# Optimization experiments

Hardware: AMD Instinct MI355X
Metric: run time of the kernel (lower is better)

The kernel has to match this reference:

```python
import jax, jax.numpy as jnp
import numpy as np

N_NODES = 100000
N_EDGES = 500000
HIDDEN = 256


def setup_inputs() -> dict:
    key = jax.random.key(0)
    k_x, k_e, k_w1, k_b1, k_w2, k_b2 = jax.random.split(key, 6)
    x = jax.random.normal(k_x, (N_NODES, HIDDEN), dtype=jnp.float32)
    edge_label_index = jax.random.randint(k_e, (2, N_EDGES), 0, N_NODES, dtype=jnp.int64)
    # fc1: Linear(2*hidden -> hidden); fc2: Linear(hidden -> 1). PyTorch stores W as [out, in].
    bound1 = 1.0 / np.sqrt(2 * HIDDEN)
    W1 = jax.random.uniform(k_w1, (HIDDEN, 2 * HIDDEN), dtype=jnp.float32, minval=-bound1, maxval=bound1)
    b1 = jax.random.uniform(k_b1, (HIDDEN,), dtype=jnp.float32, minval=-bound1, maxval=bound1)
    bound2 = 1.0 / np.sqrt(HIDDEN)
    W2 = jax.random.uniform(k_w2, (1, HIDDEN), dtype=jnp.float32, minval=-bound2, maxval=bound2)
    b2 = jax.random.uniform(k_b2, (1,), dtype=jnp.float32, minval=-bound2, maxval=bound2)
    return {"x": x, "edge_label_index": edge_label_index, "W1": W1, "b1": b1, "W2": W2, "b2": b2}


def reference(x, edge_label_index, W1, b1, W2, b2):
    # Gather endpoint features: [E, H] each
    feat_src = x[edge_label_index[0]]
    feat_dst = x[edge_label_index[1]]
    h = jnp.concatenate([feat_src, feat_dst], axis=1)  # [E, 2H]
    h = jax.nn.relu(h @ W1.T + b1)                      # [E, H]
    out = jax.nn.sigmoid(h @ W2.T + b2)                 # [E, 1]
    return out.reshape(-1)
```

## Files before the change

kernel.cpp:

```cpp
#include <hip/hip_runtime.h>
#include <math.h>

#define NNODES 100000
#define MT     64
#define NTILES 1563
#define NODESP (NTILES * MT)
#define NEDGES 500000
#define HID    256
#define K2     512
#define GEMM_GRID 256

typedef _Float16 h8v __attribute__((ext_vector_type(8)));
typedef _Float16 h2v __attribute__((ext_vector_type(2)));
typedef __bf16   bf16x8 __attribute__((ext_vector_type(8)));
typedef float    f32x4  __attribute__((ext_vector_type(4)));

__device__ __forceinline__ unsigned short f2bf(float f) {
    unsigned int u = __float_as_uint(f);
    u += 0x7FFFu + ((u >> 16) & 1u);
    return (unsigned short)(u >> 16);
}

__global__ void cvt_w1h(const float* __restrict__ W1, _Float16* __restrict__ Bsw) {
    int t = blockIdx.x * 256 + threadIdx.x;
    if (t >= 8 * 32 * 64) return;
    int lane = t & 63, nt = (t >> 6) & 31, kt = t >> 11;
    int j = nt * 16 + (lane & 15);
    int k = kt * 32 + ((lane >> 4) << 3);
    const float* src = W1 + (size_t)(j & 255) * K2 + ((j >> 8) << 8) + k;
    union { _Float16 s[8]; uint4 v; } u;
#pragma unroll
    for (int jj = 0; jj < 8; ++jj) u.s[jj] = (_Float16)src[jj];
    ((uint4*)Bsw)[t] = u.v;
}

__global__ void cvt_w2p(const float* __restrict__ W2, float* __restrict__ w2p) {
    int t = threadIdx.x;
    int i = (t >> 2) & 15, nt = t & 3;
    w2p[t] = W2[(t & ~63) | (nt * 16 + i)];
}

__global__ __launch_bounds__(512, 2) void node_gemm4(
    const float* __restrict__ x,
    const _Float16* __restrict__ Bsw,
    const float* __restrict__ b1,
    _Float16* __restrict__ UV)
{
    __shared__ __align__(16) _Float16 Asw[2048 * 8];
    const int tid  = threadIdx.x;
    const int lane = tid & 63;
    const int wave = tid >> 6;

    const h8v* B8 = (const h8v*)Bsw;
    h8v barr[8][4];
#pragma unroll
    for (int ks = 0; ks < 8; ++ks)
#pragma unroll
        for (int nt = 0; nt < 4; ++nt)
            barr[ks][nt] = B8[((size_t)(ks * 32 + wave * 4 + nt)) * 64 + lane];

    float b1v[4];
#pragma unroll
    for (int nt = 0; nt < 4; ++nt) {
        int col = wave * 64 + nt * 16 + (lane & 15);
        b1v[nt] = (col < 256) ? b1[col] : 0.0f;
    }

    uint4* A4 = (uint4*)Asw;
    const h8v* A8 = (const h8v*)Asw;
    const int k8  = tid & 31;
    const int mh  = tid >> 5;
    const int ktl = k8 >> 2, q = k8 & 3;

    auto stage = [&](int tile) {
#pragma unroll
        for (int i = 0; i < 4; ++i) {
            int m   = i * 16 + mh;
            int row = tile * MT + m;
            int rl  = row < NNODES ? row : 0;
            const float4* p = (const float4*)(x + (size_t)rl * 256 + k8 * 8);
            float4 a = p[0], b = p[1];
            union { _Float16 s[8]; uint4 v; } u;
            u.s[0] = (_Float16)a.x; u.s[1] = (_Float16)a.y;
            u.s[2] = (_Float16)a.z; u.s[3] = (_Float16)a.w;
            u.s[4] = (_Float16)b.x; u.s[5] = (_Float16)b.y;
            u.s[6] = (_Float16)b.z; u.s[7] = (_Float16)b.w;
            int logical = (ktl << 8) + ((m >> 4) << 6) + (q << 4) + (m & 15);
            A4[logical ^ ktl] = u.v;
        }
    };

    f32x4 acc[4][4] = {};
    int tile = blockIdx.x;
    if (tile >= NTILES) return;
    stage(tile);
    __syncthreads();

    while (true) {
#pragma unroll
        for (int ks = 0; ks < 8; ++ks) {
            h8v af[4];
#pragma unroll
            for (int mt = 0; mt < 4; ++mt)
                af[mt] = A8[(((ks * 4 + mt) << 6) + lane) ^ ks];
#pragma unroll
            for (int mt = 0; mt < 4; ++mt)
#pragma unroll
                for (int nt = 0; nt < 4; ++nt)
                    acc[mt][nt] = __builtin_amdgcn_mfma_f32_16x16x32_f16(
                        af[mt], barr[ks][nt], acc[mt][nt], 0, 0, 0);
        }
        __syncthreads();

        int next = tile + GEMM_GRID;
        if (next < NTILES) stage(next);

#pragma unroll
        for (int mt = 0; mt < 4; ++mt) {
#pragma unroll
            for (int r = 0; r < 4; ++r) {
                int row = tile * MT + mt * 16 + ((lane >> 4) << 2) + r;
                union { _Float16 h[4]; uint2 v; } pk;
#pragma unroll
                for (int nt = 0; nt < 4; ++nt)
                    pk.h[nt] = (_Float16)(acc[mt][nt][r] + b1v[nt]);
                *(uint2*)(UV + (size_t)row * 512 + wave * 64 + (lane & 15) * 4) = pk.v;
            }
        }
#pragma unroll
        for (int mt = 0; mt < 4; ++mt)
#pragma unroll
            for (int nt = 0; nt < 4; ++nt)
                acc[mt][nt] = f32x4{0.f, 0.f, 0.f, 0.f};

        if (next >= NTILES) break;
        tile = next;
        __syncthreads();
    }
}

__global__ __launch_bounds__(256) void edge_out4(
    const _Float16* __restrict__ UV,
    const int* __restrict__ ei,
    const float* __restrict__ w2p,
    const float* __restrict__ b2,
    float* __restrict__ out)
{
    const int tid = threadIdx.x;
    const int q   = tid & 31;
    const int g   = tid >> 5;
    const long e  = (long)blockIdx.x * 32 + g * 4;

    int4 s4 = *(const int4*)(ei + e);
    int4 d4 = *(const int4*)(ei + NEDGES + e);

    h2v w2h[4];
    {
        const float4* pw = (const float4*)w2p + q * 2;
        float4 c = pw[0], d = pw[1];
        w2h[0] = h2v{(_Float16)c.x, (_Float16)c.y};
        w2h[1] = h2v{(_Float16)c.z, (_Float16)c.w};
        w2h[2] = h2v{(_Float16)d.x, (_Float16)d.y};
        w2h[3] = h2v{(_Float16)d.z, (_Float16)d.w};
    }

    union U8 { uint4 v; h2v h[4]; };
    const _Float16* up = UV + q * 8;

    U8 uu[4], vv[4];
    uu[0].v = *(const uint4*)(up + (size_t)s4.x * 512);
    vv[0].v = *(const uint4*)(up + (size_t)d4.x * 512 + 256);
    uu[1].v = *(const uint4*)(up + (size_t)s4.y * 512);
    vv[1].v = *(const uint4*)(up + (size_t)d4.y * 512 + 256);
    uu[2].v = *(const uint4*)(up + (size_t)s4.z * 512);
    vv[2].v = *(const uint4*)(up + (size_t)d4.z * 512 + 256);
    uu[3].v = *(const uint4*)(up + (size_t)s4.w * 512);
    vv[3].v = *(const uint4*)(up + (size_t)d4.w * 512 + 256);

    const h2v zz = {(_Float16)0.0f, (_Float16)0.0f};
    float z[4] = {0.f, 0.f, 0.f, 0.f};
#pragma unroll
    for (int ed = 0; ed < 4; ++ed) {
#pragma unroll
        for (int p = 0; p < 4; ++p) {
            h2v h = uu[ed].h[p] + vv[ed].h[p];
            h = __builtin_elementwise_max(h, zz);
            z[ed] = __builtin_amdgcn_fdot2(h, w2h[p], z[ed], false);
        }
    }
#pragma unroll
    for (int m = 1; m < 32; m <<= 1) {
        z[0] += __shfl_xor(z[0], m, 32);
        z[1] += __shfl_xor(z[1], m, 32);
        z[2] += __shfl_xor(z[2], m, 32);
        z[3] += __shfl_xor(z[3], m, 32);
    }
    if (q < 4) {
        float zq = (q == 0) ? z[0] : (q == 1) ? z[1] : (q == 2) ? z[2] : z[3];
        out[e + q] = 1.0f / (1.0f + expf(-(zq + b2[0])));
    }
}

__global__ void cvt_w1_r1(const float* __restrict__ W1, unsigned short* __restrict__ Bsw) {
    int t = blockIdx.x * 256 + threadIdx.x;
    if (t >= 16 * 16 * 64) return;
    int lane = t & 63, nt = (t >> 6) & 15, kt = t >> 10;
    int n = nt * 16 + (lane & 15);
    int k = kt * 32 + ((lane >> 4) << 3);
    const float* src = W1 + (size_t)n * K2 + k;
    union { unsigned short s[8]; uint4 v; } u;
#pragma unroll
    for (int j = 0; j < 8; ++j) u.s[j] = f2bf(src[j]);
    ((uint4*)Bsw)[t] = u.v;
}

__global__ __launch_bounds__(256) void edge_mlp_fb(
    const float* __restrict__ xf, const int* __restrict__ ei,
    const unsigned short* __restrict__ Bsw, const float* __restrict__ b1,
    const float* __restrict__ W2, const float* __restrict__ b2,
    float* __restrict__ out)
{
    __shared__ __align__(16) unsigned short Asw[8 * 4 * 64 * 8];
    __shared__ float es[64];
    const int tid = threadIdx.x, lane = tid & 63, wave = tid >> 6;
    const int e0 = blockIdx.x * 64;
    if (tid < 64) es[tid] = 0.0f;
    f32x4 acc[4][4] = {};
    const bf16x8* A8 = (const bf16x8*)Asw;
    const bf16x8* B8 = (const bf16x8*)Bsw;
    for (int h = 0; h < 2; ++h) {
#pragma unroll
        for (int i = 0; i < 8; ++i) {
            int m = i * 8 + wave * 2 + (lane >> 5);
            int e = e0 + m;
            int ee = (e < NEDGES) ? e : 0;
            int node = ei[(size_t)h * NEDGES + ee];
            int chunk = lane & 31;
            const float4* p = (const float4*)(xf + ((size_t)node << 8) + (chunk << 3));
            float4 a = p[0], bq = p[1];
            union { unsigned short s[8]; uint4 v4; } u;
            u.s[0] = f2bf(a.x);  u.s[1] = f2bf(a.y);  u.s[2] = f2bf(a.z);  u.s[3] = f2bf(a.w);
            u.s[4] = f2bf(bq.x); u.s[5] = f2bf(bq.y); u.s[6] = f2bf(bq.z); u.s[7] = f2bf(bq.w);
            int ktl = chunk >> 2, qq = chunk & 3;
            int u16 = ((ktl * 4 + (m >> 4)) << 6) + (qq << 4) + (m & 15);
            u16 ^= (u16 >> 8) & 7;
            ((uint4*)Asw)[u16] = u.v4;
        }
        __syncthreads();
#pragma unroll
        for (int kt = 0; kt < 8; ++kt) {
            bf16x8 af[4], bfr[4];
#pragma unroll
            for (int mt = 0; mt < 4; ++mt) {
                int u16 = ((kt * 4 + mt) << 6) + lane;
                u16 ^= (u16 >> 8) & 7;
                af[mt] = A8[u16];
            }
#pragma unroll
            for (int nt = 0; nt < 4; ++nt)
                bfr[nt] = B8[(((h * 8 + kt) << 4) + (wave << 2) + nt) * 64 + lane];
#pragma unroll
            for (int mt = 0; mt < 4; ++mt)
#pragma unroll
                for (int nt = 0; nt < 4; ++nt)
                    acc[mt][nt] = __builtin_amdgcn_mfma_f32_16x16x32_bf16(
                        af[mt], bfr[nt], acc[mt][nt], 0, 0, 0);
        }
        __syncthreads();
    }
    float w2v[4], b1v[4];
#pragma unroll
    for (int nt = 0; nt < 4; ++nt) {
        int n = (wave << 6) + (nt << 4) + (lane & 15);
        w2v[nt] = W2[n]; b1v[nt] = b1[n];
    }
#pragma unroll
    for (int mt = 0; mt < 4; ++mt) {
#pragma unroll
        for (int r = 0; r < 4; ++r) {
            float p = 0.0f;
#pragma unroll
            for (int nt = 0; nt < 4; ++nt) {
                float hv = acc[mt][nt][r] + b1v[nt];
                p = fmaf(fmaxf(hv, 0.0f), w2v[nt], p);
            }
            p += __shfl_xor(p, 1, 16);
            p += __shfl_xor(p, 2, 16);
            p += __shfl_xor(p, 4, 16);
            p += __shfl_xor(p, 8, 16);
            if ((lane & 15) == 0)
                atomicAdd(&es[(mt << 4) + ((lane >> 4) << 2) + r], p);
        }
    }
    __syncthreads();
    if (tid < 64) {
        int e = e0 + tid;
        if (e < NEDGES) out[e] = 1.0f / (1.0f + expf(-(es[tid] + b2[0])));
    }
}

extern "C" void kernel_launch(void* const* d_in, const int* in_sizes, int n_in,
                              void* d_out, int out_size, void* d_ws, size_t ws_size,
                              hipStream_t stream) {
    const float* x  = (const float*)d_in[0];
    const int*   ei = (const int*)d_in[1];
    const float* W1 = (const float*)d_in[2];
    const float* b1 = (const float*)d_in[3];
    const float* W2 = (const float*)d_in[4];
    const float* b2 = (const float*)d_in[5];
    float* out = (float*)d_out;

    const size_t BSW_BYTES = 1 << 18;
    const size_t W2P_BYTES = 4096;
    const size_t UV_BYTES  = (size_t)NODESP * K2 * 2;
    const size_t NEED_A = BSW_BYTES + W2P_BYTES + UV_BYTES;

    if (ws_size >= NEED_A) {
        _Float16* Bsw = (_Float16*)d_ws;
        float*    w2p = (float*)((char*)d_ws + BSW_BYTES);
        _Float16* UV  = (_Float16*)((char*)d_ws + BSW_BYTES + W2P_BYTES);
        cvt_w1h<<<64, 256, 0, stream>>>(W1, Bsw);
        cvt_w2p<<<1, 256, 0, stream>>>(W2, w2p);
        node_gemm4<<<GEMM_GRID, 512, 0, stream>>>(x, Bsw, b1, UV);
        edge_out4<<<NEDGES / 32, 256, 0, stream>>>(UV, ei, w2p, b2, out);
    } else {
        unsigned short* Bsw = (unsigned short*)d_ws;
        cvt_w1_r1<<<64, 256, 0, stream>>>(W1, Bsw);
        edge_mlp_fb<<<(NEDGES + 63) / 64, 256, 0, stream>>>(x, ei, Bsw, b1, W2, b2, out);
    }
}
```

Before: 252.6 us.

## Double-buffer node GEMM A tiles and prefetch next tile into registers

The node GEMM now issues the global loads for the next x tile into registers before running the MFMA loop on the current tile. It then writes them to a second LDS buffer. This lets global memory latency overlap with compute and drops one barrier per iteration. In exchange it uses twice the LDS and 32 more VGPRs for the prefetched float4 values, which may hurt occupancy under the 512x2 launch bounds.

```diff
diff --git a/kernel.cpp b/kernel.cpp
--- a/kernel.cpp
+++ b/kernel.cpp
@@ -40,13 +40,13 @@
     w2p[t] = W2[(t & ~63) | (nt * 16 + i)];
 }
 
-__global__ __launch_bounds__(512, 2) void node_gemm4(
+__global__ __launch_bounds__(512, 2) void node_gemm5(
     const float* __restrict__ x,
     const _Float16* __restrict__ Bsw,
     const float* __restrict__ b1,
     _Float16* __restrict__ UV)
 {
-    __shared__ __align__(16) _Float16 Asw[2048 * 8];
+    __shared__ __align__(16) _Float16 Asw[2][2048 * 8];
     const int tid  = threadIdx.x;
     const int lane = tid & 63;
     const int wave = tid >> 6;
@@ -66,37 +66,53 @@
         b1v[nt] = (col < 256) ? b1[col] : 0.0f;
     }
 
-    uint4* A4 = (uint4*)Asw;
-    const h8v* A8 = (const h8v*)Asw;
     const int k8  = tid & 31;
     const int mh  = tid >> 5;
     const int ktl = k8 >> 2, q = k8 & 3;
 
-    auto stage = [&](int tile) {
+    int tile = blockIdx.x;
+    if (tile >= NTILES) return;
+
+    float4 xa[4], xb[4];
+
+    auto load_tile = [&](int t) {
 #pragma unroll
         for (int i = 0; i < 4; ++i) {
-            int m   = i * 16 + mh;
-            int row = tile * MT + m;
+            int row = t * MT + i * 16 + mh;
             int rl  = row < NNODES ? row : 0;
             const float4* p = (const float4*)(x + (size_t)rl * 256 + k8 * 8);
-            float4 a = p[0], b = p[1];
+            xa[i] = p[0];
+            xb[i] = p[1];
+        }
+    };
+    auto put_tile = [&](int buf) {
+        uint4* A4 = (uint4*)Asw[buf];
+#pragma unroll
+        for (int i = 0; i < 4; ++i) {
+            int m = i * 16 + mh;
             union { _Float16 s[8]; uint4 v; } u;
-            u.s[0] = (_Float16)a.x; u.s[1] = (_Float16)a.y;
-            u.s[2] = (_Float16)a.z; u.s[3] = (_Float16)a.w;
-            u.s[4] = (_Float16)b.x; u.s[5] = (_Float16)b.y;
-            u.s[6] = (_Float16)b.z; u.s[7] = (_Float16)b.w;
+            u.s[0] = (_Float16)xa[i].x; u.s[1] = (_Float16)xa[i].y;
+            u.s[2] = (_Float16)xa[i].z; u.s[3] = (_Float16)xa[i].w;
+            u.s[4] = (_Float16)xb[i].x; u.s[5] = (_Float16)xb[i].y;
+            u.s[6] = (_Float16)xb[i].z; u.s[7] = (_Float16)xb[i].w;
             int logical = (ktl << 8) + ((m >> 4) << 6) + (q << 4) + (m & 15);
             A4[logical ^ ktl] = u.v;
         }
     };
 
+    load_tile(tile);
+    put_tile(0);
+    __syncthreads();
+
     f32x4 acc[4][4] = {};
-    int tile = blockIdx.x;
-    if (tile >= NTILES) return;
-    stage(tile);
-    __syncthreads();
-
+    int cur = 0;
     while (true) {
+        int next = tile + GEMM_GRID;
+        bool have_next = next < NTILES;
+
+        if (have_next) load_tile(next);
+
+        const h8v* A8 = (const h8v*)Asw[cur];
 #pragma unroll
         for (int ks = 0; ks < 8; ++ks) {
             h8v af[4];
@@ -110,10 +126,8 @@
                     acc[mt][nt] = __builtin_amdgcn_mfma_f32_16x16x32_f16(
                         af[mt], barr[ks][nt], acc[mt][nt], 0, 0, 0);
         }
-        __syncthreads();
-
-        int next = tile + GEMM_GRID;
-        if (next < NTILES) stage(next);
+
+        if (have_next) put_tile(cur ^ 1);
 
 #pragma unroll
         for (int mt = 0; mt < 4; ++mt) {
@@ -133,9 +147,10 @@
             for (int nt = 0; nt < 4; ++nt)
                 acc[mt][nt] = f32x4{0.f, 0.f, 0.f, 0.f};
 
-        if (next >= NTILES) break;
+        if (!have_next) break;
+        __syncthreads();
         tile = next;
-        __syncthreads();
+        cur ^= 1;
     }
 }
 
@@ -321,7 +336,7 @@
         _Float16* UV  = (_Float16*)((char*)d_ws + BSW_BYTES + W2P_BYTES);
         cvt_w1h<<<64, 256, 0, stream>>>(W1, Bsw);
         cvt_w2p<<<1, 256, 0, stream>>>(W2, w2p);
-        node_gemm4<<<GEMM_GRID, 512, 0, stream>>>(x, Bsw, b1, UV);
+        node_gemm5<<<GEMM_GRID, 512, 0, stream>>>(x, Bsw, b1, UV);
         edge_out4<<<NEDGES / 32, 256, 0, stream>>>(UV, ei, w2p, b2, out);
     } else {
         unsigned short* Bsw = (unsigned short*)d_ws;
```

After: 261.8 us. 1.04x slower.

## Double-buffer node GEMM with direct global-to-LDS loads and 32-row tiles

Applied to the files above, without the earlier changes.

The node GEMM now copies fp32 rows of x straight into LDS with global_load_lds, using an XOR swizzle on the source address. It converts them to fp16 only when building the MFMA operands. The tile shrinks to 32 rows, and two LDS buffers let the next tile's load overlap the current tile's MFMA work. This aims to hide global-load latency and drop the register round trip used for staging. In exchange, LDS use doubles, occupancy drops to one block per CU, and correctness relies on the barrier waiting for the asynchronous LDS loads.

```diff
diff --git a/kernel.cpp b/kernel.cpp
--- a/kernel.cpp
+++ b/kernel.cpp
@@ -9,6 +9,8 @@
 #define HID    256
 #define K2     512
 #define GEMM_GRID 256
+#define MT2    32
+#define NT2    3125
 
 typedef _Float16 h8v __attribute__((ext_vector_type(8)));
 typedef _Float16 h2v __attribute__((ext_vector_type(2)));
@@ -19,6 +21,14 @@
     unsigned int u = __float_as_uint(f);
     u += 0x7FFFu + ((u >> 16) & 1u);
     return (unsigned short)(u >> 16);
+}
+
+__device__ __forceinline__ void gload16(const float* g, const float* lds_base_uniform) {
+    typedef const __attribute__((address_space(1))) unsigned int ga_u32;
+    typedef __attribute__((address_space(3))) unsigned int lds_u32;
+    __builtin_amdgcn_global_load_lds((ga_u32*)(uintptr_t)g,
+                                     (lds_u32*)(unsigned int)(uintptr_t)lds_base_uniform,
+                                     16, 0, 0);
 }
 
 __global__ void cvt_w1h(const float* __restrict__ W1, _Float16* __restrict__ Bsw) {
@@ -40,13 +50,14 @@
     w2p[t] = W2[(t & ~63) | (nt * 16 + i)];
 }
 
-__global__ __launch_bounds__(512, 2) void node_gemm4(
+__global__ __launch_bounds__(512, 1) void node_gemm8(
     const float* __restrict__ x,
     const _Float16* __restrict__ Bsw,
     const float* __restrict__ b1,
     _Float16* __restrict__ UV)
 {
-    __shared__ __align__(16) _Float16 Asw[2048 * 8];
+    __shared__ __align__(16) float A0[MT2 * 256];
+    __shared__ __align__(16) float A1[MT2 * 256];
     const int tid  = threadIdx.x;
     const int lane = tid & 63;
     const int wave = tid >> 6;
@@ -66,60 +77,43 @@
         b1v[nt] = (col < 256) ? b1[col] : 0.0f;
     }
 
-    uint4* A4 = (uint4*)Asw;
-    const h8v* A8 = (const h8v*)Asw;
-    const int k8  = tid & 31;
-    const int mh  = tid >> 5;
-    const int ktl = k8 >> 2, q = k8 & 3;
-
-    auto stage = [&](int tile) {
+    auto stage = [&](int t, float* dstb) {
 #pragma unroll
         for (int i = 0; i < 4; ++i) {
-            int m   = i * 16 + mh;
-            int row = tile * MT + m;
-            int rl  = row < NNODES ? row : 0;
-            const float4* p = (const float4*)(x + (size_t)rl * 256 + k8 * 8);
-            float4 a = p[0], b = p[1];
-            union { _Float16 s[8]; uint4 v; } u;
-            u.s[0] = (_Float16)a.x; u.s[1] = (_Float16)a.y;
-            u.s[2] = (_Float16)a.z; u.s[3] = (_Float16)a.w;
-            u.s[4] = (_Float16)b.x; u.s[5] = (_Float16)b.y;
-            u.s[6] = (_Float16)b.z; u.s[7] = (_Float16)b.w;
-            int logical = (ktl << 8) + ((m >> 4) << 6) + (q << 4) + (m & 15);
-            A4[logical ^ ktl] = u.v;
+            int row = wave * 4 + i;
+            int u   = lane ^ (row & 7);
+            const float* src = x + (size_t)(t * MT2 + row) * 256 + u * 4;
+            gload16(src, dstb + row * 256);
         }
     };
 
-    f32x4 acc[4][4] = {};
-    int tile = blockIdx.x;
-    if (tile >= NTILES) return;
-    stage(tile);
-    __syncthreads();
-
-    while (true) {
+    auto work = [&](const float* Ab, int t) {
+        const f32x4* A4 = (const f32x4*)Ab;
+        f32x4 acc[2][4] = {};
 #pragma unroll
         for (int ks = 0; ks < 8; ++ks) {
-            h8v af[4];
-#pragma unroll
-            for (int mt = 0; mt < 4; ++mt)
-                af[mt] = A8[(((ks * 4 + mt) << 6) + lane) ^ ks];
-#pragma unroll
-            for (int mt = 0; mt < 4; ++mt)
+            h8v af[2];
+#pragma unroll
+            for (int mt = 0; mt < 2; ++mt) {
+                int row = mt * 16 + (lane & 15);
+                int u0  = ks * 8 + ((lane >> 4) << 1);
+                f32x4 lo = A4[row * 64 + ( u0      ^ (row & 7))];
+                f32x4 hi = A4[row * 64 + ((u0 + 1) ^ (row & 7))];
+                af[mt] = h8v{(_Float16)lo[0], (_Float16)lo[1], (_Float16)lo[2], (_Float16)lo[3],
+                             (_Float16)hi[0], (_Float16)hi[1], (_Float16)hi[2], (_Float16)hi[3]};
+            }
+#pragma unroll
+            for (int mt = 0; mt < 2; ++mt)
 #pragma unroll
                 for (int nt = 0; nt < 4; ++nt)
                     acc[mt][nt] = __builtin_amdgcn_mfma_f32_16x16x32_f16(
                         af[mt], barr[ks][nt], acc[mt][nt], 0, 0, 0);
         }
-        __syncthreads();
-
-        int next = tile + GEMM_GRID;
-        if (next < NTILES) stage(next);
-
-#pragma unroll
-        for (int mt = 0; mt < 4; ++mt) {
+#pragma unroll
+        for (int mt = 0; mt < 2; ++mt) {
 #pragma unroll
             for (int r = 0; r < 4; ++r) {
-                int row = tile * MT + mt * 16 + ((lane >> 4) << 2) + r;
+                int row = t * MT2 + mt * 16 + ((lane >> 4) << 2) + r;
                 union { _Float16 h[4]; uint2 v; } pk;
 #pragma unroll
                 for (int nt = 0; nt < 4; ++nt)
@@ -127,15 +121,25 @@
                 *(uint2*)(UV + (size_t)row * 512 + wave * 64 + (lane & 15) * 4) = pk.v;
             }
         }
-#pragma unroll
-        for (int mt = 0; mt < 4; ++mt)
-#pragma unroll
-            for (int nt = 0; nt < 4; ++nt)
-                acc[mt][nt] = f32x4{0.f, 0.f, 0.f, 0.f};
-
-        if (next >= NTILES) break;
-        tile = next;
+    };
+
+    int tile = blockIdx.x;
+    stage(tile, A0);
+    __syncthreads();
+
+    for (;;) {
+        int n1 = tile + GEMM_GRID;
+        if (n1 < NT2) stage(n1, A1);
+        work(A0, tile);
+        if (n1 >= NT2) return;
         __syncthreads();
+
+        int n2 = n1 + GEMM_GRID;
+        if (n2 < NT2) stage(n2, A0);
+        work(A1, n1);
+        if (n2 >= NT2) return;
+        __syncthreads();
+        tile = n2;
     }
 }
 
@@ -321,7 +325,7 @@
         _Float16* UV  = (_Float16*)((char*)d_ws + BSW_BYTES + W2P_BYTES);
         cvt_w1h<<<64, 256, 0, stream>>>(W1, Bsw);
         cvt_w2p<<<1, 256, 0, stream>>>(W2, w2p);
-        node_gemm4<<<GEMM_GRID, 512, 0, stream>>>(x, Bsw, b1, UV);
+        node_gemm8<<<GEMM_GRID, 512, 0, stream>>>(x, Bsw, b1, UV);
         edge_out4<<<NEDGES / 32, 256, 0, stream>>>(UV, ei, w2p, b2, out);
     } else {
         unsigned short* Bsw = (unsigned short*)d_ws;
```

Result: faster. 243.7 us (-3.5%).
